# Optimization experiments

Measured on AMD Instinct MI355X. Metric: run time of the kernel, lower is better.

The kernel has to match this reference:

```python
import jax, jax.numpy as jnp
import numpy as np


def setup_inputs() -> dict:
    key = jax.random.key(0)
    ks = jax.random.split(key, 11)
    B, E, R, D = 2048, 20000, 500, 256
    inp = {
        "h": jax.random.uniform(ks[0], (B, E), dtype=jnp.float32),
        "t": jax.random.uniform(ks[1], (B, E), dtype=jnp.float32),
        "r": jax.random.uniform(ks[2], (B, R), dtype=jnp.float32),
        "W_er": jax.random.normal(ks[3], (D, E), dtype=jnp.float32) * 0.02,
        "W_ei": jax.random.normal(ks[4], (D, E), dtype=jnp.float32) * 0.02,
        "W_ej": jax.random.normal(ks[5], (D, E), dtype=jnp.float32) * 0.02,
        "W_ek": jax.random.normal(ks[6], (D, E), dtype=jnp.float32) * 0.02,
        "W_rr": jax.random.normal(ks[7], (D, R), dtype=jnp.float32) * 0.02,
        "W_ri": jax.random.normal(ks[8], (D, R), dtype=jnp.float32) * 0.02,
        "W_rj": jax.random.normal(ks[9], (D, R), dtype=jnp.float32) * 0.02,
        "W_rk": jax.random.normal(ks[10], (D, R), dtype=jnp.float32) * 0.02,
    }
    return inp


def reference(h, t, r, W_er, W_ei, W_ej, W_ek, W_rr, W_ri, W_rj, W_rk):
    # entity / relation projections (nn.Linear, no bias): x @ W^T -> [B, D]
    H_r, H_i, H_j, H_k = h @ W_er.T, h @ W_ei.T, h @ W_ej.T, h @ W_ek.T
    T_r, T_i, T_j, T_k = t @ W_er.T, t @ W_ei.T, t @ W_ej.T, t @ W_ek.T
    R_r, R_i, R_j, R_k = r @ W_rr.T, r @ W_ri.T, r @ W_rj.T, r @ W_rk.T

    # hypercomplex norm per row: sqrt(|R_r|^2 + |R_i|^2 + |R_j|^2 + |R_k|^2) -> [B,1]
    norm = jnp.sqrt(
        jnp.sum(R_r * R_r + R_i * R_i + R_j * R_j + R_k * R_k, axis=1, keepdims=True)
    )
    R_r, R_i, R_j, R_k = norm * R_r, norm * R_i, norm * R_j, norm * R_k

    # Hamilton product H (x) R
    Q_r = H_r * R_r - H_i * R_i - H_j * R_j - H_k * R_k
    Q_i = H_r * R_i + H_i * R_r + H_j * R_k - H_k * R_j
    Q_j = H_r * R_j - H_i * R_k + H_j * R_r + H_k * R_i
    Q_k = H_r * R_k + H_i * R_j - H_j * R_i + H_k * R_r

    # diag(Q @ T^T) == rowwise dot sum(Q*T, axis=1) -- O(B*d) form of the anti-pattern
    score = jnp.sum(Q_r * T_r + Q_i * T_i + Q_j * T_j + Q_k * T_k, axis=1, keepdims=True)
    return jax.nn.sigmoid(score)
```

## Files before the change

kernel.cpp:

```cpp
#include <hip/hip_runtime.h>


using bf16x8 = __attribute__((ext_vector_type(8))) short;
using f32x4  = __attribute__((ext_vector_type(4))) float;
using f32x16 = __attribute__((ext_vector_type(16))) float;

#define DEVINL static __device__ __forceinline__

DEVINL void split2(float x0, float x1, unsigned& h, unsigned& l) {
  unsigned u0 = __float_as_uint(x0), u1 = __float_as_uint(x1);
  unsigned h0 = u0 & 0xFFFF0000u, h1 = u1 & 0xFFFF0000u;
  h = (u0 >> 16) | h1;
  float r0 = x0 - __uint_as_float(h0);
  float r1 = x1 - __uint_as_float(h1);
  l = (__float_as_uint(r0) >> 16) | (__float_as_uint(r1) & 0xFFFF0000u);
}

DEVINL void gload16(const void* g, void* l) {
  __builtin_amdgcn_global_load_lds(
      (const __attribute__((address_space(1))) unsigned*)g,
      (__attribute__((address_space(3))) unsigned*)l, 16, 0, 0);
}

DEVINL void conv_body(const float* srow, int srcK, int kt, int rb,
                      char* dst, int ktiles, float ld[64][36], int t)
{
  {
    int r = t >> 2, kc = (t & 3) * 8;
    int k0 = kt * 32 + kc;
    const float* s = srow + (size_t)r * srcK;
    float4 v0, v1;
    if (k0 + 8 <= srcK) {
      v0 = *(const float4*)(s + k0);
      v1 = *(const float4*)(s + k0 + 4);
    } else {
      float x[8];
#pragma unroll
      for (int j = 0; j < 8; ++j) x[j] = (k0 + j < srcK) ? s[k0 + j] : 0.f;
      v0 = make_float4(x[0], x[1], x[2], x[3]);
      v1 = make_float4(x[4], x[5], x[6], x[7]);
    }
    *(float4*)&ld[r][kc]     = v0;
    *(float4*)&ld[r][kc + 4] = v1;
  }
  __syncthreads();
  {
    int g = t >> 7, s = (t >> 6) & 1, kh = (t >> 5) & 1, r31 = t & 31;
    int row = g * 32 + r31;
    int k = s * 16 + kh * 8;
    float x[8];
#pragma unroll
    for (int j = 0; j < 8; ++j) x[j] = ld[row][k + j];
    unsigned hh[4], llv[4];
    split2(x[0], x[1], hh[0], llv[0]);
    split2(x[2], x[3], hh[1], llv[1]);
    split2(x[4], x[5], hh[2], llv[2]);
    split2(x[6], x[7], hh[3], llv[3]);
    int tile_rt = rb >> 2;
    int gbase = (rb & 3) * 2;
    char* base = dst + ((size_t)tile_rt * ktiles + kt) * 32768
               + (gbase + g) * 2048 + s * 1024 + kh * 512 + r31 * 16;
    *(uint4*)base           = make_uint4(hh[0], hh[1], hh[2], hh[3]);
    *(uint4*)(base + 16384) = make_uint4(llv[0], llv[1], llv[2], llv[3]);
  }
}

__global__ void convert_img2(const float* __restrict__ src0,
                             const float* __restrict__ src1, int rows0,
                             int srcK, char* __restrict__ dst, int ktiles)
{
  __shared__ float ld[64][36];
  const int kt = blockIdx.x, rb = blockIdx.y, t = threadIdx.x;
  int row0 = rb * 64;
  const float* srow = (row0 < rows0) ? (src0 + (size_t)row0 * srcK)
                                     : (src1 + (size_t)(row0 - rows0) * srcK);
  conv_body(srow, srcK, kt, rb, dst, ktiles, ld, t);
}

__global__ void convert_q4(const float* __restrict__ p0, const float* __restrict__ p1,
                           const float* __restrict__ p2, const float* __restrict__ p3,
                           int rbPerQ, int srcK, char* __restrict__ dst,
                           size_t qStride, int ktiles)
{
  __shared__ float ld[64][36];
  const int kt = blockIdx.x, t = threadIdx.x;
  const int q = blockIdx.y / rbPerQ, rb = blockIdx.y % rbPerQ;
  const float* src = (q == 0) ? p0 : (q == 1) ? p1 : (q == 2) ? p2 : p3;
  conv_body(src + (size_t)(rb * 64) * srcK, srcK, kt, rb,
            dst + (size_t)q * qStride, ktiles, ld, t);
}

__global__ __launch_bounds__(512, 1) void gemm_ring(
    const char* __restrict__ Aimg, const char* __restrict__ Bimg, int ktiles,
    float* __restrict__ C, int MT, int NT, int KS, int swz)
{
  __shared__ __align__(16) char smem[131072];
  const int bid = blockIdx.x;

  int mt, nt, ks;
  if (swz) {
    int x = bid & 7, w = bid >> 3;
    nt = w & 3;
    int g = x + (w >> 2) * 8;
    mt = g & 15; ks = g >> 4;
  } else {
    nt = bid % NT; int q = bid / NT; mt = q % MT; ks = q / MT;
  }

  const int kt0 = (ktiles * ks) / KS;
  const int kt1 = (ktiles * (ks + 1)) / KS;
  const int nsteps = 2 * (kt1 - kt0);

  const char* Ab = Aimg + ((size_t)mt * ktiles + kt0) * 32768;
  const char* Bb = Bimg + ((size_t)nt * ktiles + kt0) * 32768;

  const int wid = threadIdx.x >> 6, lane = threadIdx.x & 63;
  const int wr = wid >> 2, wc = wid & 3;

  f32x16 acc[4][2];
#pragma unroll
  for (int mb = 0; mb < 4; ++mb)
#pragma unroll
    for (int nb = 0; nb < 2; ++nb)
#pragma unroll
      for (int e = 0; e < 16; ++e) acc[mb][nb][e] = 0.f;

#define STAGE(S)                                                               \
  {                                                                            \
    char* slot_ = smem + ((S) & 3) * 32768;                                    \
    const char* At_ = Ab + (size_t)((S) >> 1) * 32768;                         \
    const char* Bt_ = Bb + (size_t)((S) >> 1) * 32768;                         \
    const int ko_ = ((S) & 1) * 1024;                                          \
    _Pragma("unroll")                                                          \
    for (int i = 0; i < 2; ++i) {                                              \
      int p_ = 2 * wid + i;                                                    \
      int src_ = (p_ >> 3) * 16384 + (p_ & 7) * 2048 + ko_ + lane * 16;        \
      gload16(At_ + src_, slot_ + p_ * 1024);                                  \
      gload16(Bt_ + src_, slot_ + 16384 + p_ * 1024);                          \
    }                                                                          \
  }
#define COMPUTE(S)                                                             \
  {                                                                            \
    const char* slot_ = smem + ((S) & 3) * 32768;                              \
    bf16x8 a_[4][2], b_[2][2];                                                 \
    _Pragma("unroll")                                                          \
    for (int mb = 0; mb < 4; ++mb)                                             \
      _Pragma("unroll")                                                        \
      for (int pl = 0; pl < 2; ++pl)                                           \
        a_[mb][pl] = *(const bf16x8*)(slot_ + (pl * 8 + wr * 4 + mb) * 1024    \
                                      + lane * 16);                            \
    _Pragma("unroll")                                                          \
    for (int nb = 0; nb < 2; ++nb)                                             \
      _Pragma("unroll")                                                        \
      for (int pl = 0; pl < 2; ++pl)                                           \
        b_[nb][pl] = *(const bf16x8*)(slot_ + 16384                            \
                                      + (pl * 8 + wc * 2 + nb) * 1024         \
                                      + lane * 16);                            \
    __builtin_amdgcn_s_setprio(1);                                             \
    _Pragma("unroll")                                                          \
    for (int mb = 0; mb < 4; ++mb)                                             \
      _Pragma("unroll")                                                        \
      for (int nb = 0; nb < 2; ++nb) {                                         \
        f32x16* c_ = &acc[mb][nb];                                             \
        *c_ = __builtin_amdgcn_mfma_f32_32x32x16_bf16(a_[mb][0], b_[nb][0], *c_, 0, 0, 0); \
        *c_ = __builtin_amdgcn_mfma_f32_32x32x16_bf16(a_[mb][1], b_[nb][0], *c_, 0, 0, 0); \
        *c_ = __builtin_amdgcn_mfma_f32_32x32x16_bf16(a_[mb][0], b_[nb][1], *c_, 0, 0, 0); \
      }                                                                        \
    __builtin_amdgcn_s_setprio(0);                                             \
  }

  STAGE(0); STAGE(1); STAGE(2);
  asm volatile("s_waitcnt vmcnt(8)" ::: "memory");
  __builtin_amdgcn_sched_barrier(0);
  __builtin_amdgcn_s_barrier();

  int s = 0;
  for (; s + 3 < nsteps; ++s) {
    STAGE(s + 3);
    __builtin_amdgcn_sched_barrier(0);
    COMPUTE(s);
    __builtin_amdgcn_sched_barrier(0);
    asm volatile("s_waitcnt vmcnt(8)" ::: "memory");
    __builtin_amdgcn_s_barrier();
  }
  COMPUTE(s);
  __builtin_amdgcn_sched_barrier(0);
  asm volatile("s_waitcnt vmcnt(4)" ::: "memory");
  __builtin_amdgcn_s_barrier();
  ++s;
  COMPUTE(s);
  __builtin_amdgcn_sched_barrier(0);
  asm volatile("s_waitcnt vmcnt(0)" ::: "memory");
  __builtin_amdgcn_s_barrier();
  ++s;
  COMPUTE(s);
#undef STAGE
#undef COMPUTE

  float* Cb = C + (size_t)ks * (size_t)(MT * 256) * 1024;
  const long rowbase = (long)mt * 256 + wr * 128 + 4 * (lane >> 5);
  const long colbase = (long)nt * 256 + wc * 64 + (lane & 31);
#pragma unroll
  for (int mb = 0; mb < 4; ++mb)
#pragma unroll
    for (int nb = 0; nb < 2; ++nb)
#pragma unroll
      for (int reg = 0; reg < 16; ++reg) {
        long row = rowbase + mb * 32 + (reg & 3) + 8 * (reg >> 2);
        long col = colbase + nb * 32;
        Cb[(size_t)row * 1024 + col] = acc[mb][nb][reg];
      }
}

__global__ __launch_bounds__(256) void epilogue_v4(
    const float* __restrict__ C1, const float* __restrict__ C2,
    float* __restrict__ out, int KS1, int KS2)
{
  const int w = threadIdx.x >> 6, lane = threadIdx.x & 63;
  const int b = blockIdx.x * 4 + w;
  const size_t SZ1 = 4096ull * 1024ull;
  const size_t SZ2 = 2048ull * 1024ull;
  const int c4 = lane * 4;

  float H[4][4], T[4][4], R[4][4];
#pragma unroll
  for (int q = 0; q < 4; ++q) {
    float4 hv = make_float4(0.f, 0.f, 0.f, 0.f);
    float4 tv = make_float4(0.f, 0.f, 0.f, 0.f);
    float4 rv = make_float4(0.f, 0.f, 0.f, 0.f);
    for (int ks = 0; ks < KS1; ++ks) {
      float4 a = *(const float4*)(C1 + ks * SZ1 + (size_t)b * 1024 + q * 256 + c4);
      float4 c = *(const float4*)(C1 + ks * SZ1 + (size_t)(b + 2048) * 1024 + q * 256 + c4);
      hv.x += a.x; hv.y += a.y; hv.z += a.z; hv.w += a.w;
      tv.x += c.x; tv.y += c.y; tv.z += c.z; tv.w += c.w;
    }
    for (int ks = 0; ks < KS2; ++ks) {
      float4 a = *(const float4*)(C2 + ks * SZ2 + (size_t)b * 1024 + q * 256 + c4);
      rv.x += a.x; rv.y += a.y; rv.z += a.z; rv.w += a.w;
    }
    H[q][0] = hv.x; H[q][1] = hv.y; H[q][2] = hv.z; H[q][3] = hv.w;
    T[q][0] = tv.x; T[q][1] = tv.y; T[q][2] = tv.z; T[q][3] = tv.w;
    R[q][0] = rv.x; R[q][1] = rv.y; R[q][2] = rv.z; R[q][3] = rv.w;
  }

  float ss = 0.f, nn = 0.f;
#pragma unroll
  for (int j = 0; j < 4; ++j) {
    float Hr = H[0][j], Hi = H[1][j], Hj = H[2][j], Hk = H[3][j];
    float Tr = T[0][j], Ti = T[1][j], Tj = T[2][j], Tk = T[3][j];
    float Rr = R[0][j], Ri = R[1][j], Rj = R[2][j], Rk = R[3][j];
    nn += Rr*Rr + Ri*Ri + Rj*Rj + Rk*Rk;
    float Qr = Hr*Rr - Hi*Ri - Hj*Rj - Hk*Rk;
    float Qi = Hr*Ri + Hi*Rr + Hj*Rk - Hk*Rj;
    float Qj = Hr*Rj - Hi*Rk + Hj*Rr + Hk*Ri;
    float Qk = Hr*Rk + Hi*Rj - Hj*Ri + Hk*Rr;
    ss += Qr*Tr + Qi*Ti + Qj*Tj + Qk*Tk;
  }
#pragma unroll
  for (int o = 32; o; o >>= 1) {
    ss += __shfl_xor(ss, o);
    nn += __shfl_xor(nn, o);
  }
  if (lane == 0) {
    float score = sqrtf(nn) * ss;
    out[b] = 1.f / (1.f + expf(-score));
  }
}

__global__ void convert_b16(const float* __restrict__ src, int srcK,
                            char* __restrict__ dst)
{
  const int tile = blockIdx.x;
  const int wrow = threadIdx.x;
  char* base = dst + (size_t)tile * 32768;
  const float* srow = src + (size_t)wrow * srcK;
#pragma unroll
  for (int kc8 = 0; kc8 < 4; ++kc8) {
    int k0 = tile * 32 + kc8 * 8;
    float x[8];
    if (k0 + 8 <= srcK) {
      float4 v0 = *(const float4*)(srow + k0);
      float4 v1 = *(const float4*)(srow + k0 + 4);
      x[0] = v0.x; x[1] = v0.y; x[2] = v0.z; x[3] = v0.w;
      x[4] = v1.x; x[5] = v1.y; x[6] = v1.z; x[7] = v1.w;
    } else {
#pragma unroll
      for (int j = 0; j < 8; ++j) x[j] = (k0 + j < srcK) ? srow[k0 + j] : 0.f;
    }
    unsigned hh[4], ll[4];
    split2(x[0], x[1], hh[0], ll[0]);
    split2(x[2], x[3], hh[1], ll[1]);
    split2(x[4], x[5], hh[2], ll[2]);
    split2(x[6], x[7], hh[3], ll[3]);
    int lchunk = (wrow & 15) + kc8 * 16;
    int n16 = wrow >> 4;
    *(uint4*)(base + (size_t)n16 * 1024 + lchunk * 16)         = make_uint4(hh[0], hh[1], hh[2], hh[3]);
    *(uint4*)(base + 16384 + (size_t)n16 * 1024 + lchunk * 16) = make_uint4(ll[0], ll[1], ll[2], ll[3]);
  }
}

__global__ void pad_r(const float* __restrict__ src, float* __restrict__ dst)
{
  int row = blockIdx.y;
  int k = threadIdx.x * 4;
  float4 v = make_float4(0.f, 0.f, 0.f, 0.f);
  if (k + 3 < 500) v = *(const float4*)(src + (size_t)row * 500 + k);
  *(float4*)(dst + (size_t)row * 512 + k) = v;
}

__global__ __launch_bounds__(512, 2) void gemm3p(
    const float* __restrict__ A0, const float* __restrict__ A1, int mtA0, long lda,
    const char* __restrict__ Bimg, int ktilesTot,
    float* __restrict__ C, long ldc, int MT, int NT, int KS, int swz)
{
  extern __shared__ char smemd[];
  const int tid = threadIdx.x;
  const int bid = blockIdx.x;

  int mt, nt, ks;
  if (swz) {
    int x = bid & 7, w = bid >> 3;
    nt = w & 3;
    int g = x + (w >> 2) * 8;
    mt = g & 15; ks = g >> 4;
  } else {
    nt = bid % NT; int q = bid / NT; mt = q % MT; ks = q / MT;
  }

  const int kt0 = (ktilesTot * ks) / KS;
  const int kt1 = (ktilesTot * (ks + 1)) / KS;

  const float* Ablk = (mt < mtA0) ? (A0 + (size_t)mt * 256 * lda)
                                  : (A1 + (size_t)(mt - mtA0) * 256 * lda);
  const char* Bt = Bimg + ((size_t)nt * ktilesTot + kt0) * 32768;

  const int wid = tid >> 6, lane = tid & 63;
  const int wr = wid >> 2, wc = wid & 3;
  const int l15 = lane & 15, lq = lane >> 4;

  const float* aSrc = Ablk + (size_t)(wid * 32 + (lane >> 3)) * lda
                      + (size_t)kt0 * 32 + 4 * (lane & 7);

  int awoff[4];
  {
    int kg = (lane & 7) >> 1, half = lane & 1;
#pragma unroll
    for (int i = 0; i < 4; ++i) {
      int m15 = (lane >> 3) + 8 * (i & 1);
      awoff[i] = (2 * wid + (i >> 1)) * 2048 + (((m15 ^ kg) + kg * 16) << 4) + half * 8;
    }
  }
  const int aroff = (((l15 ^ lq) + lq * 16) << 4);
  const int bbase = 32768 + (wc * 4) * 1024 + lane * 16;

  f32x4 acc[8][4];
#pragma unroll
  for (int m = 0; m < 8; ++m)
#pragma unroll
    for (int j = 0; j < 4; ++j)
#pragma unroll
      for (int e = 0; e < 4; ++e) acc[m][j][e] = 0.f;

  float4 aR[4];

#define ISSUE_A(KT)                                                            \
  {                                                                            \
    const float* p_ = aSrc + (size_t)((KT) - kt0) * 32;                        \
    _Pragma("unroll")                                                          \
    for (int i = 0; i < 4; ++i) aR[i] = *(const float4*)(p_ + (size_t)(8 * i) * lda); \
  }
#define ISSUE_B(DST, KT)                                                       \
  {                                                                            \
    const char* p_ = Bt + (size_t)((KT) - kt0) * 32768 + wid * 4096 + lane * 16; \
    _Pragma("unroll")                                                          \
    for (int i = 0; i < 4; ++i)                                                \
      gload16(p_ + i * 1024, (DST) + 32768 + wid * 4096 + i * 1024);           \
  }
#define WRITE_A(DST)                                                           \
  {                                                                            \
    _Pragma("unroll")                                                          \
    for (int i = 0; i < 4; ++i) {                                              \
      unsigned h0_, l0_, h1_, l1_;                                             \
      split2(aR[i].x, aR[i].y, h0_, l0_);                                      \
      split2(aR[i].z, aR[i].w, h1_, l1_);                                      \
      *(uint2*)((DST) + awoff[i])        = make_uint2(h0_, h1_);               \
      *(uint2*)((DST) + awoff[i] + 1024) = make_uint2(l0_, l1_);               \
    }                                                                          \
  }

  ISSUE_A(kt0);
  ISSUE_B(smemd, kt0);
  WRITE_A(smemd);
  asm volatile("s_waitcnt vmcnt(0)" ::: "memory");
  asm volatile("s_waitcnt lgkmcnt(0)" ::: "memory");
  __builtin_amdgcn_s_barrier();

  for (int kt = kt0; kt < kt1; ++kt) {
    char* bufc = smemd + (size_t)((kt - kt0) & 1) * 65536;
    char* bufn = smemd + (size_t)(((kt - kt0) & 1) ^ 1) * 65536;
    const bool nx = (kt + 1 < kt1);

    if (nx) { ISSUE_A(kt + 1); ISSUE_B(bufn, kt + 1); }

    bf16x8 bh[4], bl[4];
#pragma unroll
    for (int j = 0; j < 4; ++j) {
      bh[j] = *(const bf16x8*)(bufc + bbase + j * 1024);
      bl[j] = *(const bf16x8*)(bufc + bbase + j * 1024 + 16384);
    }

    __builtin_amdgcn_s_setprio(1);
#pragma unroll
    for (int m = 0; m < 4; ++m) {
      const char* ab = bufc + (wr * 8 + m) * 2048;
      bf16x8 ah = *(const bf16x8*)(ab + aroff);
      bf16x8 al = *(const bf16x8*)(ab + aroff + 1024);
#pragma unroll
      for (int j = 0; j < 4; ++j) {
        acc[m][j] = __builtin_amdgcn_mfma_f32_16x16x32_bf16(ah, bh[j], acc[m][j], 0, 0, 0);
        acc[m][j] = __builtin_amdgcn_mfma_f32_16x16x32_bf16(al, bh[j], acc[m][j], 0, 0, 0);
        acc[m][j] = __builtin_amdgcn_mfma_f32_16x16x32_bf16(ah, bl[j], acc[m][j], 0, 0, 0);
      }
    }
    __builtin_amdgcn_s_setprio(0);

    __builtin_amdgcn_sched_barrier(0);
    if (nx) WRITE_A(bufn);

    __builtin_amdgcn_s_setprio(1);
#pragma unroll
    for (int m = 4; m < 8; ++m) {
      const char* ab = bufc + (wr * 8 + m) * 2048;
      bf16x8 ah = *(const bf16x8*)(ab + aroff);
      bf16x8 al = *(const bf16x8*)(ab + aroff + 1024);
#pragma unroll
      for (int j = 0; j < 4; ++j) {
        acc[m][j] = __builtin_amdgcn_mfma_f32_16x16x32_bf16(ah, bh[j], acc[m][j], 0, 0, 0);
        acc[m][j] = __builtin_amdgcn_mfma_f32_16x16x32_bf16(al, bh[j], acc[m][j], 0, 0, 0);
        acc[m][j] = __builtin_amdgcn_mfma_f32_16x16x32_bf16(ah, bl[j], acc[m][j], 0, 0, 0);
      }
    }
    __builtin_amdgcn_s_setprio(0);

    asm volatile("s_waitcnt vmcnt(0)" ::: "memory");
    asm volatile("s_waitcnt lgkmcnt(0)" ::: "memory");
    __builtin_amdgcn_s_barrier();
  }
#undef ISSUE_A
#undef ISSUE_B
#undef WRITE_A

  float* Cb = C + (size_t)ks * (size_t)(MT * 256) * (size_t)ldc;
  const long rowbase = (long)mt * 256 + wr * 128 + lq * 4;
  const long colbase = (long)nt * 256 + wc * 64 + l15;
#pragma unroll
  for (int m = 0; m < 8; ++m)
#pragma unroll
    for (int j = 0; j < 4; ++j)
#pragma unroll
      for (int reg = 0; reg < 4; ++reg) {
        long row = rowbase + m * 16 + reg;
        long col = colbase + j * 16;
        Cb[(size_t)row * ldc + col] = acc[m][j][reg];
      }
}

__global__ void epilogue_kernel(const float* __restrict__ C1, const float* __restrict__ C2,
                                float* __restrict__ out, int KS1, int KS2)
{
  const int b = blockIdx.x;
  const int d = threadIdx.x;
  const size_t SZ1 = 4096ull * 1024ull;
  const size_t SZ2 = 2048ull * 1024ull;

  float Hq[4], Tq[4], Rq[4];
#pragma unroll
  for (int q = 0; q < 4; ++q) {
    float hv = 0.f, tv = 0.f, rv = 0.f;
    for (int ks = 0; ks < KS1; ++ks) {
      hv += C1[ks * SZ1 + (size_t)b * 1024 + q * 256 + d];
      tv += C1[ks * SZ1 + (size_t)(b + 2048) * 1024 + q * 256 + d];
    }
    for (int ks = 0; ks < KS2; ++ks)
      rv += C2[ks * SZ2 + (size_t)b * 1024 + q * 256 + d];
    Hq[q] = hv; Tq[q] = tv; Rq[q] = rv;
  }
  float nn = Rq[0]*Rq[0] + Rq[1]*Rq[1] + Rq[2]*Rq[2] + Rq[3]*Rq[3];
  float Qr = Hq[0]*Rq[0] - Hq[1]*Rq[1] - Hq[2]*Rq[2] - Hq[3]*Rq[3];
  float Qi = Hq[0]*Rq[1] + Hq[1]*Rq[0] + Hq[2]*Rq[3] - Hq[3]*Rq[2];
  float Qj = Hq[0]*Rq[2] - Hq[1]*Rq[3] + Hq[2]*Rq[0] + Hq[3]*Rq[1];
  float Qk = Hq[0]*Rq[3] + Hq[1]*Rq[2] - Hq[2]*Rq[1] + Hq[3]*Rq[0];
  float ss = Qr*Tq[0] + Qi*Tq[1] + Qj*Tq[2] + Qk*Tq[3];

#pragma unroll
  for (int o = 32; o; o >>= 1) {
    ss += __shfl_xor(ss, o);
    nn += __shfl_xor(nn, o);
  }
  __shared__ float red[8];
  int lane = d & 63, w = d >> 6;
  if (lane == 0) { red[w] = ss; red[4 + w] = nn; }
  __syncthreads();
  if (d == 0) {
    float S = red[0] + red[1] + red[2] + red[3];
    float N = red[4] + red[5] + red[6] + red[7];
    float score = sqrtf(N) * S;
    out[b] = 1.f / (1.f + expf(-score));
  }
}

extern "C" void kernel_launch(void* const* d_in, const int* in_sizes, int n_in,
                              void* d_out, int out_size, void* d_ws, size_t ws_size,
                              hipStream_t stream)
{
  const float* h = (const float*)d_in[0];
  const float* t = (const float*)d_in[1];
  const float* r = (const float*)d_in[2];
  const float* We[4] = {(const float*)d_in[3], (const float*)d_in[4],
                        (const float*)d_in[5], (const float*)d_in[6]};
  const float* Wr[4] = {(const float*)d_in[7], (const float*)d_in[8],
                        (const float*)d_in[9], (const float*)d_in[10]};
  float* out = (float*)d_out;
  char* ws = (char*)d_ws;

  const size_t offA  = 0;
  const size_t offB  = 327680000;
  const size_t offWr = offB + 81920000;
  const size_t offRi = offWr + 2097152;
  const size_t offC1 = offRi + 4194304;
  const size_t C1sz  = 4096ull * 1024ull * 4ull;
  const size_t C2sz  = 2048ull * 1024ull * 4ull;
  const size_t needImg = offC1 + 4 * C1sz;

  if (ws_size >= needImg) {
    float* C1 = (float*)(ws + offC1);
    float* C2 = (float*)(ws + offB);
    const int KS2 = 8;

    convert_img2<<<dim3(625, 64), 256, 0, stream>>>(h, t, 2048, 20000, ws + offA, 625);
    convert_q4<<<dim3(625, 16), 256, 0, stream>>>(
        We[0], We[1], We[2], We[3], 4, 20000, ws + offB, (size_t)625 * 32768, 625);
    convert_q4<<<dim3(16, 16), 256, 0, stream>>>(
        Wr[0], Wr[1], Wr[2], Wr[3], 4, 500, ws + offWr, (size_t)16 * 32768, 16);
    convert_img2<<<dim3(16, 32), 256, 0, stream>>>(r, r, 2048, 500, ws + offRi, 16);

    gemm_ring<<<dim3(256), 512, 0, stream>>>(
        ws + offA, ws + offB, 625, C1, 16, 4, 4, 1);
    gemm_ring<<<dim3(8 * 4 * KS2), 512, 0, stream>>>(
        ws + offRi, ws + offWr, 16, C2, 8, 4, KS2, 0);

    epilogue_v4<<<dim3(512), 256, 0, stream>>>(C1, C2, out, 4, KS2);
    return;
  }

  const size_t fB  = 0;
  const size_t fWr = 81920000;
  const size_t fR  = fWr + 2097152;
  const size_t fC1 = fR + 4194304;
  const int KS = (ws_size >= fC1 + 4 * C1sz + 8388608ull) ? 4 : 2;
  const size_t fC2 = fC1 + (size_t)KS * C1sz;

  float* rpad = (float*)(ws + fR);
  float* C1   = (float*)(ws + fC1);
  float* C2   = (float*)(ws + fC2);

  for (int q = 0; q < 4; ++q) {
    convert_b16<<<dim3(625), 256, 0, stream>>>(We[q], 20000, ws + fB + (size_t)q * 625 * 32768);
    convert_b16<<<dim3(16), 256, 0, stream>>>(Wr[q], 500, ws + fWr + (size_t)q * 16 * 32768);
  }
  pad_r<<<dim3(1, 2048), 128, 0, stream>>>(r, rpad);

  gemm3p<<<dim3(16 * 4 * KS), 512, 131072, stream>>>(
      h, t, 8, 20000L, (const char*)(ws + fB), 625,
      C1, 1024L, 16, 4, KS, KS == 4 ? 1 : 0);
  gemm3p<<<dim3(32), 512, 131072, stream>>>(
      rpad, rpad, 8, 512L, (const char*)(ws + fWr), 16,
      C2, 1024L, 8, 4, 1, 0);

  epilogue_kernel<<<dim3(2048), 256, 0, stream>>>(C1, C2, out, KS, 1);
}
```

Baseline: 574.7 us.

## Add 256-thread 4-wave GEMM kernel with larger per-wave tiles and 4-slot ring

Adds a new GEMM kernel for the main entity projection that uses 256 threads (4 waves) instead of 512. Each wave computes a 4x4 grid of 32x32 MFMA tiles, so it keeps more accumulators and reuses more operands from registers. The k-tile is split into half-steps that stream through a 4-slot LDS ring with direct global-to-LDS loads three stages ahead, and MFMA sections are raised in priority with setprio. The aim is to cut LDS read traffic per FLOP and synchronisation overhead, at the cost of heavy register pressure (256 accumulator floats per thread) and fewer waves to hide latency.

Result: no change. 585.2 us (+1.8%).

```diff
diff --git a/kernel.cpp b/kernel.cpp
--- a/kernel.cpp
+++ b/kernel.cpp
@@ -88,6 +88,129 @@
   const float* src = (q == 0) ? p0 : (q == 1) ? p1 : (q == 2) ? p2 : p3;
   conv_body(src + (size_t)(rb * 64) * srcK, srcK, kt, rb,
             dst + (size_t)q * qStride, ktiles, ld, t);
+}
+
+__global__ __launch_bounds__(256, 1) void gemm_fring(
+    const char* __restrict__ Aimg, const char* __restrict__ Bimg, int ktiles,
+    float* __restrict__ C, int MT, int NT, int KS, int swz)
+{
+  __shared__ __align__(16) char smem[131072];
+  const int bid = blockIdx.x;
+
+  int mt, nt, ks;
+  if (swz) {
+    int x = bid & 7, w = bid >> 3;
+    nt = w & 3;
+    int g = x + (w >> 2) * 8;
+    mt = g & 15; ks = g >> 4;
+  } else {
+    nt = bid % NT; int q = bid / NT; mt = q % MT; ks = q / MT;
+  }
+
+  const int kt0 = (ktiles * ks) / KS;
+  const int kt1 = (ktiles * (ks + 1)) / KS;
+  const int nsteps = 2 * (kt1 - kt0);
+
+  const char* Ab = Aimg + ((size_t)mt * ktiles + kt0) * 32768;
+  const char* Bb = Bimg + ((size_t)nt * ktiles + kt0) * 32768;
+
+  const int wid = threadIdx.x >> 6, lane = threadIdx.x & 63;
+  const int wr = wid >> 1, wc = wid & 1;
+
+  f32x16 acc[4][4];
+#pragma unroll
+  for (int mb = 0; mb < 4; ++mb)
+#pragma unroll
+    for (int nb = 0; nb < 4; ++nb)
+#pragma unroll
+      for (int e = 0; e < 16; ++e) acc[mb][nb][e] = 0.f;
+
+#define STAGE(S)                                                               \
+  {                                                                            \
+    char* slot_ = smem + ((S) & 3) * 32768;                                    \
+    const char* At_ = Ab + (size_t)((S) >> 1) * 32768;                         \
+    const char* Bt_ = Bb + (size_t)((S) >> 1) * 32768;                         \
+    const int ko_ = ((S) & 1) * 1024;                                          \
+    _Pragma("unroll")                                                          \
+    for (int i = 0; i < 4; ++i) {                                              \
+      int p_ = 4 * wid + i;                                                    \
+      int src_ = (p_ >> 3) * 16384 + (p_ & 7) * 2048 + ko_ + lane * 16;        \
+      gload16(At_ + src_, slot_ + p_ * 1024);                                  \
+      gload16(Bt_ + src_, slot_ + 16384 + p_ * 1024);                          \
+    }                                                                          \
+  }
+#define COMPUTE(S)                                                             \
+  {                                                                            \
+    const char* slot_ = smem + ((S) & 3) * 32768;                              \
+    bf16x8 a_[4][2], b_[4][2];                                                 \
+    _Pragma("unroll")                                                          \
+    for (int mb = 0; mb < 4; ++mb)                                             \
+      _Pragma("unroll")                                                        \
+      for (int pl = 0; pl < 2; ++pl)                                           \
+        a_[mb][pl] = *(const bf16x8*)(slot_ + (pl * 8 + wr * 4 + mb) * 1024    \
+                                      + lane * 16);                            \
+    _Pragma("unroll")                                                          \
+    for (int nb = 0; nb < 4; ++nb)                                             \
+      _Pragma("unroll")                                                        \
+      for (int pl = 0; pl < 2; ++pl)                                           \
+        b_[nb][pl] = *(const bf16x8*)(slot_ + 16384                            \
+                                      + (pl * 8 + wc * 4 + nb) * 1024         \
+                                      + lane * 16);                            \
+    __builtin_amdgcn_s_setprio(1);                                             \
+    _Pragma("unroll")                                                          \
+    for (int p = 0; p < 3; ++p)                                                \
+      _Pragma("unroll")                                                        \
+      for (int mb = 0; mb < 4; ++mb)                                           \
+        _Pragma("unroll")                                                      \
+        for (int nb = 0; nb < 4; ++nb) {                                       \
+          bf16x8 av = (p == 1) ? a_[mb][1] : a_[mb][0];                        \
+          bf16x8 bv = (p == 2) ? b_[nb][1] : b_[nb][0];                        \
+          acc[mb][nb] = __builtin_amdgcn_mfma_f32_32x32x16_bf16(av, bv, acc[mb][nb], 0, 0, 0); \
+        }                                                                      \
+    __builtin_amdgcn_s_setprio(0);                                             \
+  }
+
+  STAGE(0); STAGE(1); STAGE(2);
+  asm volatile("s_waitcnt vmcnt(16)" ::: "memory");
+  __builtin_amdgcn_sched_barrier(0);
+  __builtin_amdgcn_s_barrier();
+
+  int s = 0;
+  for (; s + 3 < nsteps; ++s) {
+    STAGE(s + 3);
+    __builtin_amdgcn_sched_barrier(0);
+    COMPUTE(s);
+    __builtin_amdgcn_sched_barrier(0);
+    asm volatile("s_waitcnt vmcnt(16)" ::: "memory");
+    __builtin_amdgcn_s_barrier();
+  }
+  COMPUTE(s);
+  __builtin_amdgcn_sched_barrier(0);
+  asm volatile("s_waitcnt vmcnt(8)" ::: "memory");
+  __builtin_amdgcn_s_barrier();
+  ++s;
+  COMPUTE(s);
+  __builtin_amdgcn_sched_barrier(0);
+  asm volatile("s_waitcnt vmcnt(0)" ::: "memory");
+  __builtin_amdgcn_s_barrier();
+  ++s;
+  COMPUTE(s);
+#undef STAGE
+#undef COMPUTE
+
+  float* Cb = C + (size_t)ks * (size_t)(MT * 256) * 1024;
+  const long rowbase = (long)mt * 256 + wr * 128 + 4 * (lane >> 5);
+  const long colbase = (long)nt * 256 + wc * 128 + (lane & 31);
+#pragma unroll
+  for (int mb = 0; mb < 4; ++mb)
+#pragma unroll
+    for (int nb = 0; nb < 4; ++nb)
+#pragma unroll
+      for (int reg = 0; reg < 16; ++reg) {
+        long row = rowbase + mb * 32 + (reg & 3) + 8 * (reg >> 2);
+        long col = colbase + nb * 32;
+        Cb[(size_t)row * 1024 + col] = acc[mb][nb][reg];
+      }
 }
 
 __global__ __launch_bounds__(512, 1) void gemm_ring(
@@ -544,7 +667,7 @@
         Wr[0], Wr[1], Wr[2], Wr[3], 4, 500, ws + offWr, (size_t)16 * 32768, 16);
     convert_img2<<<dim3(16, 32), 256, 0, stream>>>(r, r, 2048, 500, ws + offRi, 16);
 
-    gemm_ring<<<dim3(256), 512, 0, stream>>>(
+    gemm_fring<<<dim3(256), 256, 0, stream>>>(
         ws + offA, ws + offB, 625, C1, 16, 4, 4, 1);
     gemm_ring<<<dim3(8 * 4 * KS2), 512, 0, stream>>>(
         ws + offRi, ws + offWr, 16, C2, 8, 4, KS2, 0);
```
